# Performance work log

Hardware: AMD Instinct MI355X
Metric: run time of the kernel (lower is better)

## Reference

```python
import jax, jax.numpy as jnp
import numpy as np

CAUSAL = True

def setup_inputs() -> dict:
    key = jax.random.key(0)
    kq, kk, kv = jax.random.split(key, 3)
    B, S, H, D = 2, 2048, 16, 64
    q = jax.random.normal(kq, (B, S, H, D), dtype=jnp.float32)
    k = jax.random.normal(kk, (B, S, H, D), dtype=jnp.float32)
    v = jax.random.normal(kv, (B, S, H, D), dtype=jnp.float32)
    return {"q": q, "k": k, "v": v}

def reference(q, k, v):
    # q,k,v: [B, S, H, D]
    B, Sq, H, D = q.shape
    Sk = k.shape[1]
    scale = 1.0 / jnp.sqrt(jnp.asarray(D, dtype=q.dtype))
    # scores: [B, H, Sq, Sk]
    scores = jnp.einsum('bqhd,bkhd->bhqk', q * scale, k)
    if CAUSAL:
        causal_mask = jnp.triu(jnp.ones((Sq, Sk), dtype=bool), k=1)
        scores = jnp.where(causal_mask, -jnp.inf, scores)
    attn = jax.nn.softmax(scores, axis=-1)
    # output: [B, Sq, H, D]
    out = jnp.einsum('bhqk,bkhd->bqhd', attn, v)
    return out
```

## Files before the change

kernel.cpp:

```cpp
#include <hip/hip_runtime.h>


typedef __bf16  bf16x8_t  __attribute__((ext_vector_type(8)));
typedef short   short4_t  __attribute__((ext_vector_type(4)));
typedef float   f32x4     __attribute__((ext_vector_type(4)));

#define MFMA_K32(a, b, c) __builtin_amdgcn_mfma_f32_16x16x32_bf16((a), (b), (c), 0, 0, 0)

__device__ __forceinline__ f32x4 mfma_k16(short4_t a, short4_t b, f32x4 c) {
#if defined(__HIP_DEVICE_COMPILE__)
    return __builtin_amdgcn_mfma_f32_16x16x16bf16_1k(a, b, c, 0, 0, 0);
#else
    return c;
#endif
}

constexpr int   SEQ = 2048, NH = 16;
constexpr int   SROW = NH * 64;
constexpr float QS   = 0.125f * 1.44269504088896f;

__device__ __forceinline__ unsigned f2bfu(float f) {
    unsigned u = __builtin_bit_cast(unsigned, f);
    return (u + 0x7fffu + ((u >> 16) & 1u)) >> 16;
}
__device__ __forceinline__ unsigned pk2(float x, float y) {
#if defined(__HIP_DEVICE_COMPILE__) && __has_builtin(__builtin_amdgcn_cvt_pk_bf16_f32)
    typedef __bf16 bfv2 __attribute__((ext_vector_type(2)));
    bfv2 v = __builtin_amdgcn_cvt_pk_bf16_f32(x, y);
    return __builtin_bit_cast(unsigned, v);
#else
    return (f2bfu(x) & 0xffffu) | (f2bfu(y) << 16);
#endif
}

__global__ __launch_bounds__(256, 2) void fa_fwd(const float* __restrict__ Q,
                                                 const float* __restrict__ K,
                                                 const float* __restrict__ V,
                                                 float* __restrict__ O) {
    const int id = blockIdx.x;
    const int bh = id & 31;
    const int pr = id >> 5;
    const int b  = bh >> 4, h = bh & 15;
    const int T0 = 31 - pr;
    const int T1 = pr;

    const int tid  = threadIdx.x;
    const int wave = tid >> 6;
    const int lane = tid & 63;
    const int lhi  = lane >> 4;
    const int llo  = lane & 15;

    __shared__ __align__(16) unsigned short Kl[64][72];
    __shared__ __align__(16) unsigned short Vt[64][72];

    bf16x8_t qf[2][2];
#pragma unroll
    for (int ph = 0; ph < 2; ++ph) {
        const int Tq = ph ? T1 : T0;
#pragma unroll
        for (int ks = 0; ks < 2; ++ks) {
            const float* qp = Q + (size_t)((b * SEQ + Tq * 64 + wave * 16 + llo) * SROW + h * 64 + ks * 32 + lhi * 8);
            float4 a = ((const float4*)qp)[0], c = ((const float4*)qp)[1];
            uint4 u;
            u.x = pk2(a.x * QS, a.y * QS); u.y = pk2(a.z * QS, a.w * QS);
            u.z = pk2(c.x * QS, c.y * QS); u.w = pk2(c.z * QS, c.w * QS);
            qf[ph][ks] = __builtin_bit_cast(bf16x8_t, u);
        }
    }

    const float* Kb = K + (size_t)(b * SEQ) * SROW + h * 64;
    const float* Vb = V + (size_t)(b * SEQ) * SROW + h * 64;

    const int skr = tid >> 4;
    const int skc = tid & 15;
    const int va   = tid & 31;
    const int vc   = tid >> 5;
    const int vcol = (8 * vc + 8 * (va >> 2)) & 63;

    float4 pkf[4];
    float2 pvf[8];
#pragma unroll
    for (int p = 0; p < 4; ++p)
        pkf[p] = *(const float4*)(Kb + (size_t)(skr + 16 * p) * SROW + skc * 4);
#pragma unroll
    for (int j = 0; j < 8; ++j)
        pvf[j] = *(const float2*)(Vb + (size_t)(8 * vc + j) * SROW + 2 * va);

    f32x4 acc[4], accL;
    accL = (f32x4){0.f, 0.f, 0.f, 0.f};
#pragma unroll
    for (int dt = 0; dt < 4; ++dt) acc[dt] = (f32x4){0.f, 0.f, 0.f, 0.f};

    short4_t ones;
#pragma unroll
    for (int j = 0; j < 4; ++j) ones[j] = (short)0x3F80;

    const int split = T0 + 1;

    for (int it = 0; it < 33; ++it) {
        const int ph = (it >= split);

        if (it == split) {
            const int q0e = T0 * 64 + wave * 16;
#pragma unroll
            for (int r = 0; r < 4; ++r) {
                const float inv = 1.0f / accL[r];
                float* ob = O + (size_t)((b * SEQ + q0e + lhi * 4 + r) * SROW + h * 64);
#pragma unroll
                for (int dt = 0; dt < 4; ++dt) ob[dt * 16 + llo] = acc[dt][r] * inv;
            }
            accL = (f32x4){0.f, 0.f, 0.f, 0.f};
#pragma unroll
            for (int dt = 0; dt < 4; ++dt) acc[dt] = (f32x4){0.f, 0.f, 0.f, 0.f};
        }

        const int kt  = ph ? it - split : it;
        const int q0  = (ph ? T1 : T0) * 64 + wave * 16;
        const int kv0 = kt * 64;

        __syncthreads();

#pragma unroll
        for (int p = 0; p < 4; ++p)
            *(uint2*)&Kl[skr + 16 * p][skc * 4] =
                make_uint2(pk2(pkf[p].x, pkf[p].y), pk2(pkf[p].z, pkf[p].w));

        {
            uint4 u0, u1;
            u0.x = pk2(pvf[0].x, pvf[1].x); u0.y = pk2(pvf[2].x, pvf[3].x);
            u0.z = pk2(pvf[4].x, pvf[5].x); u0.w = pk2(pvf[6].x, pvf[7].x);
            u1.x = pk2(pvf[0].y, pvf[1].y); u1.y = pk2(pvf[2].y, pvf[3].y);
            u1.z = pk2(pvf[4].y, pvf[5].y); u1.w = pk2(pvf[6].y, pvf[7].y);
            *(uint4*)&Vt[2 * va    ][vcol] = u0;
            *(uint4*)&Vt[2 * va + 1][vcol] = u1;
        }
        __syncthreads();

        if (it + 1 < 33) {
            const int kt2 = (it + 1 >= split) ? (it + 1 - split) : (it + 1);
            const float* kb = Kb + (size_t)(kt2 * 64) * SROW;
            const float* vb = Vb + (size_t)(kt2 * 64) * SROW;
#pragma unroll
            for (int p = 0; p < 4; ++p)
                pkf[p] = *(const float4*)(kb + (size_t)(skr + 16 * p) * SROW + skc * 4);
#pragma unroll
            for (int j = 0; j < 8; ++j)
                pvf[j] = *(const float2*)(vb + (size_t)(8 * vc + j) * SROW + 2 * va);
        }

        f32x4 s[4];
#pragma unroll
        for (int nt = 0; nt < 4; ++nt) {
            bf16x8_t kf0 = *(const bf16x8_t*)&Kl[nt * 16 + llo][lhi * 8];
            bf16x8_t kf1 = *(const bf16x8_t*)&Kl[nt * 16 + llo][32 + lhi * 8];
            f32x4 z = (f32x4){0.f, 0.f, 0.f, 0.f};
            z = MFMA_K32(kf0, qf[ph][0], z);
            z = MFMA_K32(kf1, qf[ph][1], z);
            s[nt] = z;
        }

        if (kv0 + 63 > q0) {
            const int m_g = q0 + llo;
#pragma unroll
            for (int nt = 0; nt < 4; ++nt)
#pragma unroll
                for (int r = 0; r < 4; ++r)
                    if (kv0 + nt * 16 + lhi * 4 + r > m_g) s[nt][r] = -INFINITY;
        }

        short4_t pf[4];
#pragma unroll
        for (int nt = 0; nt < 4; ++nt) {
            uint2 u = make_uint2(
                pk2(__builtin_amdgcn_exp2f(s[nt][0]), __builtin_amdgcn_exp2f(s[nt][1])),
                pk2(__builtin_amdgcn_exp2f(s[nt][2]), __builtin_amdgcn_exp2f(s[nt][3])));
            pf[nt] = __builtin_bit_cast(short4_t, u);
        }

#pragma unroll
        for (int ks = 0; ks < 4; ++ks) {
#pragma unroll
            for (int dt = 0; dt < 4; ++dt) {
                const int d   = dt * 16 + llo;
                const int col = (ks * 16 + lhi * 4 + 8 * (d >> 3)) & 63;
                uint2 vu = *(const uint2*)&Vt[d][col];
                short4_t vf = __builtin_bit_cast(short4_t, vu);
                acc[dt] = mfma_k16(pf[ks], vf, acc[dt]);
            }
            accL = mfma_k16(pf[ks], ones, accL);
        }
    }

    const int q0e = T1 * 64 + wave * 16;
#pragma unroll
    for (int r = 0; r < 4; ++r) {
        const float inv = 1.0f / accL[r];
        float* ob = O + (size_t)((b * SEQ + q0e + lhi * 4 + r) * SROW + h * 64);
#pragma unroll
        for (int dt = 0; dt < 4; ++dt) ob[dt * 16 + llo] = acc[dt][r] * inv;
    }
}

extern "C" void kernel_launch(void* const* d_in, const int* in_sizes, int n_in,
                              void* d_out, int out_size, void* d_ws, size_t ws_size,
                              hipStream_t stream) {
    const float* q = (const float*)d_in[0];
    const float* k = (const float*)d_in[1];
    const float* v = (const float*)d_in[2];
    float* o = (float*)d_out;
    fa_fwd<<<dim3(512), dim3(256), 0, stream>>>(q, k, v, o);
}
```

Measured before the change: 130.7 us.

## Prepack K/V to swizzled bf16 and stream tiles via global_load_lds double buffering

```diff
diff --git a/kernel.cpp b/kernel.cpp
--- a/kernel.cpp
+++ b/kernel.cpp
@@ -33,9 +33,48 @@
 #endif
 }
 
+__global__ __launch_bounds__(256) void prepack(const float* __restrict__ K,
+                                               const float* __restrict__ V,
+                                               unsigned short* __restrict__ Kp,
+                                               unsigned short* __restrict__ Vp) {
+    const int blk = blockIdx.x;
+    if (blk < 2048) {
+        const int bh = blk >> 6, sg = blk & 63;
+        const int b  = bh >> 4,  h  = bh & 15;
+        const int sl = threadIdx.x >> 3;
+        const int c  = threadIdx.x & 7;
+        const int s  = sg * 32 + sl;
+        const float* src = K + (size_t)(b * SEQ + s) * SROW + h * 64 + c * 8;
+        float4 a = ((const float4*)src)[0], d4 = ((const float4*)src)[1];
+        uint4 u;
+        u.x = pk2(a.x, a.y);  u.y = pk2(a.z, a.w);
+        u.z = pk2(d4.x, d4.y); u.w = pk2(d4.z, d4.w);
+        *(uint4*)(Kp + ((size_t)bh * SEQ + s) * 64 + (size_t)((c ^ (s & 7)) * 8)) = u;
+    } else {
+        const int q  = blk - 2048;
+        const int bh = q >> 5, t = q & 31;
+        const int b  = bh >> 4, h = bh & 15;
+        const int d  = threadIdx.x & 63;
+        const int kg = threadIdx.x >> 6;
+        const float* src = V + (size_t)(b * SEQ + t * 64 + kg * 16) * SROW + h * 64 + d;
+        float f[16];
+#pragma unroll
+        for (int j = 0; j < 16; ++j) f[j] = src[(size_t)j * SROW];
+        uint4 u0, u1;
+        u0.x = pk2(f[0], f[1]);   u0.y = pk2(f[2], f[3]);
+        u0.z = pk2(f[4], f[5]);   u0.w = pk2(f[6], f[7]);
+        u1.x = pk2(f[8], f[9]);   u1.y = pk2(f[10], f[11]);
+        u1.z = pk2(f[12], f[13]); u1.w = pk2(f[14], f[15]);
+        const int key = (d >> 1) & 7;
+        unsigned short* row = Vp + (((size_t)bh * 32 + t) * 64 + d) * 64;
+        *(uint4*)(row + (size_t)((((kg * 2)     ^ key) * 8))) = u0;
+        *(uint4*)(row + (size_t)((((kg * 2 + 1) ^ key) * 8))) = u1;
+    }
+}
+
 __global__ __launch_bounds__(256, 2) void fa_fwd(const float* __restrict__ Q,
-                                                 const float* __restrict__ K,
-                                                 const float* __restrict__ V,
+                                                 const unsigned short* __restrict__ Kp,
+                                                 const unsigned short* __restrict__ Vp,
                                                  float* __restrict__ O) {
     const int id = blockIdx.x;
     const int bh = id & 31;
@@ -50,8 +89,8 @@
     const int lhi  = lane >> 4;
     const int llo  = lane & 15;
 
-    __shared__ __align__(16) unsigned short Kl[64][72];
-    __shared__ __align__(16) unsigned short Vt[64][72];
+    __shared__ __align__(16) unsigned short KB[2][64 * 64];
+    __shared__ __align__(16) unsigned short VB[2][64 * 64];
 
     bf16x8_t qf[2][2];
 #pragma unroll
@@ -68,23 +107,24 @@
         }
     }
 
-    const float* Kb = K + (size_t)(b * SEQ) * SROW + h * 64;
-    const float* Vb = V + (size_t)(b * SEQ) * SROW + h * 64;
-
-    const int skr = tid >> 4;
-    const int skc = tid & 15;
-    const int va   = tid & 31;
-    const int vc   = tid >> 5;
-    const int vcol = (8 * vc + 8 * (va >> 2)) & 63;
-
-    float4 pkf[4];
-    float2 pvf[8];
-#pragma unroll
-    for (int p = 0; p < 4; ++p)
-        pkf[p] = *(const float4*)(Kb + (size_t)(skr + 16 * p) * SROW + skc * 4);
-#pragma unroll
-    for (int j = 0; j < 8; ++j)
-        pvf[j] = *(const float2*)(Vb + (size_t)(8 * vc + j) * SROW + 2 * va);
+    const unsigned short* Kt = Kp + (size_t)bh * (SEQ * 64);
+    const unsigned short* Vt = Vp + (size_t)bh * (SEQ * 64);
+
+    const int ch = wave * 2;
+
+#define STAGE(kt, bufi)                                                                     \
+    do {                                                                                    \
+        const unsigned short* gk = Kt + (size_t)(kt) * 4096 + ch * 512 + lane * 8;          \
+        const unsigned short* gv = Vt + (size_t)(kt) * 4096 + ch * 512 + lane * 8;          \
+        __builtin_amdgcn_global_load_lds((const __attribute__((address_space(1))) void*)gk, \
+            (__attribute__((address_space(3))) void*)&KB[bufi][ch * 512], 16, 0, 0);        \
+        __builtin_amdgcn_global_load_lds((const __attribute__((address_space(1))) void*)(gk + 512), \
+            (__attribute__((address_space(3))) void*)&KB[bufi][ch * 512 + 512], 16, 0, 0);  \
+        __builtin_amdgcn_global_load_lds((const __attribute__((address_space(1))) void*)gv, \
+            (__attribute__((address_space(3))) void*)&VB[bufi][ch * 512], 16, 0, 0);        \
+        __builtin_amdgcn_global_load_lds((const __attribute__((address_space(1))) void*)(gv + 512), \
+            (__attribute__((address_space(3))) void*)&VB[bufi][ch * 512 + 512], 16, 0, 0);  \
+    } while (0)
 
     f32x4 acc[4], accL;
     accL = (f32x4){0.f, 0.f, 0.f, 0.f};
@@ -96,6 +136,9 @@
     for (int j = 0; j < 4; ++j) ones[j] = (short)0x3F80;
 
     const int split = T0 + 1;
+
+    STAGE(0, 0);
+    __syncthreads();
 
     for (int it = 0; it < 33; ++it) {
         const int ph = (it >= split);
@@ -118,41 +161,21 @@
         const int q0  = (ph ? T1 : T0) * 64 + wave * 16;
         const int kv0 = kt * 64;
 
-        __syncthreads();
-
-#pragma unroll
-        for (int p = 0; p < 4; ++p)
-            *(uint2*)&Kl[skr + 16 * p][skc * 4] =
-                make_uint2(pk2(pkf[p].x, pkf[p].y), pk2(pkf[p].z, pkf[p].w));
-
-        {
-            uint4 u0, u1;
-            u0.x = pk2(pvf[0].x, pvf[1].x); u0.y = pk2(pvf[2].x, pvf[3].x);
-            u0.z = pk2(pvf[4].x, pvf[5].x); u0.w = pk2(pvf[6].x, pvf[7].x);
-            u1.x = pk2(pvf[0].y, pvf[1].y); u1.y = pk2(pvf[2].y, pvf[3].y);
-            u1.z = pk2(pvf[4].y, pvf[5].y); u1.w = pk2(pvf[6].y, pvf[7].y);
-            *(uint4*)&Vt[2 * va    ][vcol] = u0;
-            *(uint4*)&Vt[2 * va + 1][vcol] = u1;
-        }
-        __syncthreads();
-
         if (it + 1 < 33) {
             const int kt2 = (it + 1 >= split) ? (it + 1 - split) : (it + 1);
-            const float* kb = Kb + (size_t)(kt2 * 64) * SROW;
-            const float* vb = Vb + (size_t)(kt2 * 64) * SROW;
-#pragma unroll
-            for (int p = 0; p < 4; ++p)
-                pkf[p] = *(const float4*)(kb + (size_t)(skr + 16 * p) * SROW + skc * 4);
-#pragma unroll
-            for (int j = 0; j < 8; ++j)
-                pvf[j] = *(const float2*)(vb + (size_t)(8 * vc + j) * SROW + 2 * va);
-        }
+            STAGE(kt2, (it + 1) & 1);
+        }
+
+        const unsigned short* Kl = KB[it & 1];
+        const unsigned short* Vl = VB[it & 1];
 
         f32x4 s[4];
 #pragma unroll
         for (int nt = 0; nt < 4; ++nt) {
-            bf16x8_t kf0 = *(const bf16x8_t*)&Kl[nt * 16 + llo][lhi * 8];
-            bf16x8_t kf1 = *(const bf16x8_t*)&Kl[nt * 16 + llo][32 + lhi * 8];
+            const int base = (nt * 16 + llo) * 64;
+            const int p0   = (lhi ^ (llo & 7)) * 8;
+            bf16x8_t kf0 = *(const bf16x8_t*)&Kl[base + p0];
+            bf16x8_t kf1 = *(const bf16x8_t*)&Kl[base + (p0 ^ 32)];
             f32x4 z = (f32x4){0.f, 0.f, 0.f, 0.f};
             z = MFMA_K32(kf0, qf[ph][0], z);
             z = MFMA_K32(kf1, qf[ph][1], z);
@@ -181,14 +204,16 @@
         for (int ks = 0; ks < 4; ++ks) {
 #pragma unroll
             for (int dt = 0; dt < 4; ++dt) {
-                const int d   = dt * 16 + llo;
-                const int col = (ks * 16 + lhi * 4 + 8 * (d >> 3)) & 63;
-                uint2 vu = *(const uint2*)&Vt[d][col];
-                short4_t vf = __builtin_bit_cast(short4_t, vu);
+                const int d = dt * 16 + llo;
+                const int u = ks * 4 + lhi;
+                const int p = (((u >> 1) ^ (llo >> 1)) * 8) + (u & 1) * 4;
+                short4_t vf = *(const short4_t*)&Vl[d * 64 + p];
                 acc[dt] = mfma_k16(pf[ks], vf, acc[dt]);
             }
             accL = mfma_k16(pf[ks], ones, accL);
         }
+
+        __syncthreads();
     }
 
     const int q0e = T1 * 64 + wave * 16;
@@ -199,6 +224,7 @@
 #pragma unroll
         for (int dt = 0; dt < 4; ++dt) ob[dt * 16 + llo] = acc[dt][r] * inv;
     }
+#undef STAGE
 }
 
 extern "C" void kernel_launch(void* const* d_in, const int* in_sizes, int n_in,
@@ -208,5 +234,8 @@
     const float* k = (const float*)d_in[1];
     const float* v = (const float*)d_in[2];
     float* o = (float*)d_out;
-    fa_fwd<<<dim3(512), dim3(256), 0, stream>>>(q, k, v, o);
-}
+    unsigned short* Kp = (unsigned short*)d_ws;
+    unsigned short* Vp = Kp + (size_t)2 * NH * SEQ * 64;
+    prepack<<<dim3(3072), dim3(256), 0, stream>>>(k, v, Kp, Vp);
+    fa_fwd<<<dim3(512), dim3(256), 0, stream>>>(q, Kp, Vp, o);
+}
```

New measurement: 137.5 us. 5.2% more time.
